# Kernel optimization log

Measured on AMD Instinct MI355X. Metric: run time of the kernel, lower is better.

The kernel has to match this reference:

```python
import jax, jax.numpy as jnp
import numpy as np

N_NODES = 100000


def _gcn_layer(x, W, b, src, dst, n):
    # PyG GCNConv with default add_self_loops=True, symmetric normalization.
    h = x @ W  # [N, out]
    deg = jax.ops.segment_sum(jnp.ones_like(dst, dtype=h.dtype), dst, num_segments=n)
    dinv = jnp.where(deg > 0, jax.lax.rsqrt(deg), 0.0)
    norm = dinv[src] * dinv[dst]  # [E]
    msg = h[src] * norm[:, None]  # gather + scale
    out = jax.ops.segment_sum(msg, dst, num_segments=n)  # scatter-add at targets
    return out + b


def setup_inputs() -> dict:
    key = jax.random.key(0)
    ks = jax.random.split(key, 8)
    n, e = N_NODES, 3200000
    x = jax.random.normal(ks[0], (n, 16), dtype=jnp.float32)
    edge_index = jax.random.randint(ks[1], (2, e), 0, n, dtype=jnp.int64)
    def glorot(k, fi, fo):
        lim = float(np.sqrt(6.0 / (fi + fo)))
        return jax.random.uniform(k, (fi, fo), jnp.float32, -lim, lim)
    return {
        "x": x,
        "edge_index": edge_index,
        "W1": glorot(ks[2], 16, 32), "b1": jnp.zeros((32,), jnp.float32),
        "W2": glorot(ks[3], 32, 64), "b2": jnp.zeros((64,), jnp.float32),
        "W3": glorot(ks[4], 64, 1),  "b3": jnp.zeros((1,), jnp.float32),
    }


def reference(x, edge_index, W1, b1, W2, b2, W3, b3):
    n = x.shape[0]
    # add self-loops once (shared by all layers)
    loops = jnp.arange(n, dtype=edge_index.dtype)
    src = jnp.concatenate([edge_index[0], loops])
    dst = jnp.concatenate([edge_index[1], loops])
    h = _gcn_layer(x, W1, b1, src, dst, n)
    h = jax.nn.relu(h)  # dropout is identity in eval mode
    h = _gcn_layer(h, W2, b2, src, dst, n)
    h = jax.nn.relu(h)
    h = _gcn_layer(h, W3, b3, src, dst, n)
    return jax.nn.sigmoid(h)
```

## Files before the change

kernel.cpp:

```cpp
#include <hip/hip_runtime.h>
#include <hip/hip_bf16.h>
#include <math.h>


#define CW    128
#define CSH   7
#define MAXBUK 1024
#define EPB   8192
#define CAP   5120

static inline int cdiv(int a, int b) { return (a + b - 1) / b; }

__device__ inline unsigned int bf16_rn(float f) {
    unsigned int u = __float_as_uint(f);
    return (u + 0x7fffu + ((u >> 16) & 1u)) >> 16;
}
#define BLO(u) __uint_as_float((u) << 16)
#define BHI(u) __uint_as_float((u) & 0xffff0000u)

#define UNPACK_ADD(A, V) \
    A[0] += BLO(V.x); A[1] += BHI(V.x); \
    A[2] += BLO(V.y); A[3] += BHI(V.y); \
    A[4] += BLO(V.z); A[5] += BHI(V.z); \
    A[6] += BLO(V.w); A[7] += BHI(V.w);
#define UNPACK_ADD2(A, V) \
    A[0] += BLO(V.x); A[1] += BHI(V.x); \
    A[2] += BLO(V.y); A[3] += BHI(V.y);


__global__ void __launch_bounds__(256) k_bscatter(const int* __restrict__ src,
                                                  const int* __restrict__ dst,
                                                  int* __restrict__ gcur,
                                                  int* __restrict__ ebuf, int e, int nbuk) {
    __shared__ int lh[MAXBUK];
    __shared__ int lo[MAXBUK];
    __shared__ int lb[MAXBUK];
    __shared__ int sh[256];
    __shared__ int stage[EPB];
    __shared__ unsigned short bkOf[EPB];
    int4 db[8];
    int t = threadIdx.x;
    for (int b = t; b < nbuk; b += 256) lh[b] = 0;
    __syncthreads();
    int base4 = blockIdx.x * (EPB / 4);
    int e4 = e >> 2;
#pragma unroll
    for (int j = 0; j < 8; j++) {
        int i4 = base4 + j * 256 + t;
        if (i4 < e4) {
            int4 d = ((const int4*)dst)[i4];
            db[j] = d;
            atomicAdd(&lh[d.x >> CSH], 1); atomicAdd(&lh[d.y >> CSH], 1);
            atomicAdd(&lh[d.z >> CSH], 1); atomicAdd(&lh[d.w >> CSH], 1);
        } else db[j] = make_int4(-1, -1, -1, -1);
    }
    __syncthreads();
    int carry = 0;
    for (int cb = 0; cb < nbuk; cb += 256) {
        int b = cb + t;
        int c = (b < nbuk) ? lh[b] : 0;
        if (b < nbuk && c) lb[b] = b * CAP + atomicAdd(&gcur[b], c);
        sh[t] = c;
        __syncthreads();
        for (int o = 1; o < 256; o <<= 1) {
            int u = (t >= o) ? sh[t - o] : 0;
            __syncthreads();
            sh[t] += u;
            __syncthreads();
        }
        if (b < nbuk) lo[b] = sh[t] - c + carry;
        carry += sh[255];
        __syncthreads();
    }
    for (int b = t; b < nbuk; b += 256) lh[b] = 0;
    __syncthreads();
#pragma unroll
    for (int j = 0; j < 8; j++) {
        int i4 = base4 + j * 256 + t;
        if (i4 < e4) {
            int4 s = ((const int4*)src)[i4];
            int4 d = db[j];
            int dd, ss, b, r, slot;
#define PUT(DX, SX) \
            dd = DX; ss = SX; b = dd >> CSH; \
            r = atomicAdd(&lh[b], 1); slot = lo[b] + r; \
            stage[slot] = ((dd & (CW - 1)) << 17) | ss; \
            bkOf[slot] = (unsigned short)b;
            PUT(d.x, s.x) PUT(d.y, s.y) PUT(d.z, s.z) PUT(d.w, s.w)
#undef PUT
        }
    }
    __syncthreads();
    int tot = min(EPB, e - blockIdx.x * EPB);
#pragma unroll
    for (int j = 0; j < 32; j++) {
        int slot = j * 256 + t;
        if (slot < tot) {
            int b = bkOf[slot];
            ebuf[lb[b] + (slot - lo[b])] = stage[slot];
        }
    }
}


__global__ void __launch_bounds__(512) k_csr2(const int* __restrict__ ebuf,
                                              const int* __restrict__ gcur,
                                              int* __restrict__ rowstart,
                                              int* __restrict__ csr_src,
                                              float* __restrict__ dinv,
                                              const float* __restrict__ x,
                                              unsigned int* __restrict__ xs,
                                              int n, int e, int nbuk) {
    __shared__ int cnt[CW];
    __shared__ int offs[CW];
    __shared__ int red[512];
    int t = threadIdx.x;
    int bid = blockIdx.x;
    int part = 0;
    for (int j = t; j < bid; j += 512) part += gcur[j];
    red[t] = part;
    __syncthreads();
    for (int o = 256; o > 0; o >>= 1) {
        if (t < o) red[t] += red[t + o];
        __syncthreads();
    }
    int dbeg = red[0];
    if (t < CW) cnt[t] = 0;
    __syncthreads();
    int cnt_b = gcur[bid];
    const int4* eb4 = (const int4*)(ebuf + (size_t)bid * CAP);
    int n4 = (cnt_b + 3) >> 2;
    for (int k4 = t; k4 < n4; k4 += 512) {
        int4 v = eb4[k4];
        int rem = cnt_b - (k4 << 2);
        atomicAdd(&cnt[v.x >> 17], 1);
        if (rem > 1) atomicAdd(&cnt[v.y >> 17], 1);
        if (rem > 2) atomicAdd(&cnt[v.z >> 17], 1);
        if (rem > 3) atomicAdd(&cnt[v.w >> 17], 1);
    }
    __syncthreads();
    int v = (t < CW) ? cnt[t] : 0;
    if (t < CW) offs[t] = v;
    __syncthreads();
    for (int o = 1; o < CW; o <<= 1) {
        int u = (t < CW && t >= o) ? offs[t - o] : 0;
        __syncthreads();
        if (t < CW) offs[t] += u;
        __syncthreads();
    }
    int node = bid * CW + t;
    if (t < CW) {
        int ex = offs[t] - v;
        float dd = rsqrtf((float)v + 1.0f);
        if (node < n) {
            rowstart[node] = dbeg + ex;
            dinv[node] = dd;
            const float4* xr = (const float4*)(x + (size_t)node * 16);
            float4 v0 = xr[0], v1 = xr[1], v2 = xr[2], v3 = xr[3];
            uint4 o0, o1;
            o0.x = bf16_rn(v0.x * dd) | (bf16_rn(v0.y * dd) << 16);
            o0.y = bf16_rn(v0.z * dd) | (bf16_rn(v0.w * dd) << 16);
            o0.z = bf16_rn(v1.x * dd) | (bf16_rn(v1.y * dd) << 16);
            o0.w = bf16_rn(v1.z * dd) | (bf16_rn(v1.w * dd) << 16);
            o1.x = bf16_rn(v2.x * dd) | (bf16_rn(v2.y * dd) << 16);
            o1.y = bf16_rn(v2.z * dd) | (bf16_rn(v2.w * dd) << 16);
            o1.z = bf16_rn(v3.x * dd) | (bf16_rn(v3.y * dd) << 16);
            o1.w = bf16_rn(v3.z * dd) | (bf16_rn(v3.w * dd) << 16);
            uint4* xo = (uint4*)(xs + (size_t)node * 8);
            xo[0] = o0; xo[1] = o1;
        }
        cnt[t] = ex;
    }
    __syncthreads();
    for (int k4 = t; k4 < n4; k4 += 512) {
        int4 vv = eb4[k4];
        int rem = cnt_b - (k4 << 2);
        int pv, r;
#define SCAT(PV) pv = PV; r = atomicAdd(&cnt[pv >> 17], 1); csr_src[dbeg + r] = pv & 0x1FFFF;
        SCAT(vv.x)
        if (rem > 1) { SCAT(vv.y) }
        if (rem > 2) { SCAT(vv.z) }
        if (rem > 3) { SCAT(vv.w) }
#undef SCAT
    }
    if (bid == 0 && t == 0) rowstart[n] = e;
}


__global__ void __launch_bounds__(256) k_pull16d(const int* __restrict__ rowstart,
                                                 const int* __restrict__ csr_src,
                                                 const float* __restrict__ dinv,
                                                 const unsigned int* __restrict__ xs,
                                                 const float* __restrict__ W1,
                                                 const float* __restrict__ b1,
                                                 unsigned int* __restrict__ h1s, int n) {
    __shared__ float sAgg[4][16];
    __shared__ float sDd[4];
    int t = threadIdx.x;
    int wv = t >> 6;
    int lane = t & 63;
    int wid = blockIdx.x * 4 + wv;
    if (wid < n) {
        int q = lane & 3;
        int beg = rowstart[wid], end = rowstart[wid + 1];
        const uint2* x2 = (const uint2*)xs;
        float dd = dinv[wid];
        uint2 sv = x2[(size_t)wid * 4 + q];
        float a0[4], a1[4], a2[4];
#pragma unroll
        for (int i = 0; i < 4; i++) { a0[i] = 0.f; a1[i] = 0.f; a2[i] = 0.f; }
        int k = beg + (lane >> 2);
        for (; k + 32 < end; k += 48) {
            int s0 = __builtin_nontemporal_load(csr_src + k);
            int s1 = __builtin_nontemporal_load(csr_src + k + 16);
            int s2 = __builtin_nontemporal_load(csr_src + k + 32);
            uint2 v0 = x2[(size_t)s0 * 4 + q];
            uint2 v1 = x2[(size_t)s1 * 4 + q];
            uint2 v2 = x2[(size_t)s2 * 4 + q];
            UNPACK_ADD2(a0, v0);
            UNPACK_ADD2(a1, v1);
            UNPACK_ADD2(a2, v2);
        }
        for (; k < end; k += 16) {
            int s0 = __builtin_nontemporal_load(csr_src + k);
            uint2 v0 = x2[(size_t)s0 * 4 + q];
            UNPACK_ADD2(a0, v0);
        }
#pragma unroll
        for (int i = 0; i < 4; i++) a0[i] += a1[i] + a2[i];
#pragma unroll
        for (int off = 4; off < 64; off <<= 1)
#pragma unroll
            for (int i = 0; i < 4; i++) a0[i] += __shfl_xor(a0[i], off);
        UNPACK_ADD2(a0, sv);
        if (lane < 4) {
#pragma unroll
            for (int i = 0; i < 4; i++) sAgg[wv][q * 4 + i] = a0[i] * dd;
            if (q == 0) sDd[wv] = dd;
        }
    }
    __syncthreads();
    if (t < 64) {
        int w2 = t >> 4, c = t & 15;
        int node = blockIdx.x * 4 + w2;
        if (node < n) {
            float dd = sDd[w2];
            const float* a = sAgg[w2];
            float o0 = b1[2 * c], o1 = b1[2 * c + 1];
#pragma unroll
            for (int k = 0; k < 16; k++) {
                float av = a[k];
                o0 += av * W1[k * 32 + 2 * c];
                o1 += av * W1[k * 32 + 2 * c + 1];
            }
            h1s[(size_t)node * 16 + c] =
                bf16_rn(fmaxf(o0, 0.f) * dd) | (bf16_rn(fmaxf(o1, 0.f) * dd) << 16);
        }
    }
}


__global__ void __launch_bounds__(256) k_pull32(const int* __restrict__ rowstart,
                                                const int* __restrict__ csr_src,
                                                const float* __restrict__ dinv,
                                                const unsigned int* __restrict__ h1s,
                                                float* __restrict__ agg32, int n) {
    int wid = (blockIdx.x * blockDim.x + threadIdx.x) >> 6;
    if (wid >= n) return;
    int lane = threadIdx.x & 63;
    int f4 = lane & 3;
    int beg = rowstart[wid], end = rowstart[wid + 1];
    const uint4* h4 = (const uint4*)h1s;
    float dd = dinv[wid];
    uint4 sv = h4[(size_t)wid * 4 + f4];
    float acc[8], ac1[8], ac2[8];
#pragma unroll
    for (int i = 0; i < 8; i++) { acc[i] = 0.f; ac1[i] = 0.f; ac2[i] = 0.f; }
    int k = beg + (lane >> 2);
    for (; k + 32 < end; k += 48) {
        int s0 = __builtin_nontemporal_load(csr_src + k);
        int s1 = __builtin_nontemporal_load(csr_src + k + 16);
        int s2 = __builtin_nontemporal_load(csr_src + k + 32);
        uint4 v0 = h4[(size_t)s0 * 4 + f4];
        uint4 v1 = h4[(size_t)s1 * 4 + f4];
        uint4 v2 = h4[(size_t)s2 * 4 + f4];
        UNPACK_ADD(acc, v0);
        UNPACK_ADD(ac1, v1);
        UNPACK_ADD(ac2, v2);
    }
    for (; k < end; k += 16) {
        int s0 = __builtin_nontemporal_load(csr_src + k);
        uint4 v0 = h4[(size_t)s0 * 4 + f4];
        UNPACK_ADD(acc, v0);
    }
#pragma unroll
    for (int i = 0; i < 8; i++) acc[i] += ac1[i] + ac2[i];
#pragma unroll
    for (int off = 4; off < 64; off <<= 1)
#pragma unroll
        for (int i = 0; i < 8; i++) acc[i] += __shfl_xor(acc[i], off);
    UNPACK_ADD(acc, sv);
    if (lane < 4) {
        float4* o4 = (float4*)(agg32 + (size_t)wid * 32 + f4 * 8);
        o4[0] = make_float4(acc[0] * dd, acc[1] * dd, acc[2] * dd, acc[3] * dd);
        o4[1] = make_float4(acc[4] * dd, acc[5] * dd, acc[6] * dd, acc[7] * dd);
    }
}


__global__ void __launch_bounds__(256) k_dense2(const float* __restrict__ agg,
                                                const float* __restrict__ dinv,
                                                const float* __restrict__ W2,
                                                const float* __restrict__ b2,
                                                const float* __restrict__ W3,
                                                float* __restrict__ t2, int n) {
    int node = blockIdx.x * 256 + threadIdx.x;
    if (node >= n) return;
    float in[32];
    const float4* a4 = (const float4*)(agg + (size_t)node * 32);
#pragma unroll
    for (int f = 0; f < 8; f++) {
        float4 v = a4[f];
        in[4 * f] = v.x; in[4 * f + 1] = v.y; in[4 * f + 2] = v.z; in[4 * f + 3] = v.w;
    }
    float p = 0.f;
#pragma unroll
    for (int cb = 0; cb < 4; cb++) {
        float o[16];
#pragma unroll
        for (int c = 0; c < 16; c++) o[c] = b2[cb * 16 + c];
#pragma unroll
        for (int k = 0; k < 32; k++) {
            float ik = in[k];
#pragma unroll
            for (int c = 0; c < 16; c++) o[c] += ik * W2[k * 64 + cb * 16 + c];
        }
#pragma unroll
        for (int c = 0; c < 16; c++) p += fmaxf(o[c], 0.f) * W3[cb * 16 + c];
    }
    t2[node] = p * dinv[node];
}


__global__ void __launch_bounds__(256) k_pull1_sig(const int* __restrict__ rowstart,
                                                   const int* __restrict__ csr_src,
                                                   const float* __restrict__ dinv,
                                                   const float* __restrict__ t2,
                                                   const float* __restrict__ b3,
                                                   float* __restrict__ out, int n) {
    int tid = blockIdx.x * blockDim.x + threadIdx.x;
    int wid = tid >> 5;
    if (wid >= n) return;
    int lane32 = threadIdx.x & 31;
    int beg = rowstart[wid], end = rowstart[wid + 1];
    float selfv = t2[wid];
    float dd = dinv[wid];
    float acc = 0.f, ac1 = 0.f;
    int k = beg + lane32;
    for (; k + 32 < end; k += 64) {
        acc += t2[__builtin_nontemporal_load(csr_src + k)];
        ac1 += t2[__builtin_nontemporal_load(csr_src + k + 32)];
    }
    if (k < end) acc += t2[__builtin_nontemporal_load(csr_src + k)];
    acc += ac1;
#pragma unroll
    for (int off = 1; off < 32; off <<= 1) acc += __shfl_xor(acc, off);
    if (lane32 == 0) {
        float v = (acc + selfv) * dd + b3[0];
        out[wid] = 1.0f / (1.0f + expf(-v));
    }
}


extern "C" void kernel_launch(void* const* d_in, const int* in_sizes, int n_in,
                              void* d_out, int out_size, void* d_ws, size_t ws_size,
                              hipStream_t stream) {
    const float* x  = (const float*)d_in[0];
    const int*   ei = (const int*)d_in[1];
    const float* W1 = (const float*)d_in[2];
    const float* b1 = (const float*)d_in[3];
    const float* W2 = (const float*)d_in[4];
    const float* b2 = (const float*)d_in[5];
    const float* W3 = (const float*)d_in[6];
    const float* b3 = (const float*)d_in[7];

    const int n = in_sizes[0] / 16;
    const int e = in_sizes[1] / 2;
    const int* src = ei;
    const int* dst = ei + e;
    const int nbuk = cdiv(n, CW);

    auto rup = [](size_t v) { return (v + 15) & ~(size_t)15; };
    char* wp = (char*)d_ws;
    auto alloc = [&](size_t elems) { void* p = wp; wp += rup(elems) * 4; return p; };
    int*   gcur     = (int*)  alloc(MAXBUK);
    float* dinv     = (float*)alloc(n);
    int*   rowstart = (int*)  alloc(n + 1);
    int*   ebuf     = (int*)  alloc((size_t)nbuk * CAP);
    int*   csr_src  = (int*)  alloc(e);
    unsigned int* xs  = (unsigned int*)alloc((size_t)8 * n);
    unsigned int* h1s = (unsigned int*)alloc((size_t)16 * n);
    float* agg32    = (float*)alloc((size_t)32 * n);
    float* t2       = (float*)alloc(n);

    float* out = (float*)d_out;
    const int B = 256;

    hipMemsetAsync(gcur, 0, MAXBUK * 4, stream);
    k_bscatter<<<cdiv(e, EPB), B, 0, stream>>>(src, dst, gcur, ebuf, e, nbuk);
    k_csr2<<<nbuk, 512, 0, stream>>>(ebuf, gcur, rowstart, csr_src,
                                     dinv, x, xs, n, e, nbuk);

    k_pull16d<<<cdiv(n, 4), B, 0, stream>>>(rowstart, csr_src, dinv, xs, W1, b1, h1s, n);

    k_pull32<<<cdiv(n * 64, B), B, 0, stream>>>(rowstart, csr_src, dinv, h1s, agg32, n);
    k_dense2<<<cdiv(n, B), B, 0, stream>>>(agg32, dinv, W2, b2, W3, t2, n);

    k_pull1_sig<<<cdiv(n * 32, B), B, 0, stream>>>(rowstart, csr_src, dinv, t2, b3, out, n);
}
```

Baseline: 215.6 us.

## Fuse layer-2 gather with dense W2/W3 projection in one kernel

Merges the 32-wide neighbour aggregation kernel and the dense layer-2/W3 projection kernel into one. Each wavefront aggregates one node, puts the result in shared memory, then has each lane compute one of the 64 outputs and reduce across the wave with shuffles. This removes the fp32 agg32 intermediate round trip through global memory and one launch. It also cuts the gather unroll from three accumulators to two, and adds a block-wide barrier plus a cross-lane reduction per node.

```diff
diff --git a/kernel.cpp b/kernel.cpp
--- a/kernel.cpp
+++ b/kernel.cpp
@@ -260,85 +260,67 @@
 }
 
 
-__global__ void __launch_bounds__(256) k_pull32(const int* __restrict__ rowstart,
-                                                const int* __restrict__ csr_src,
-                                                const float* __restrict__ dinv,
-                                                const unsigned int* __restrict__ h1s,
-                                                float* __restrict__ agg32, int n) {
-    int wid = (blockIdx.x * blockDim.x + threadIdx.x) >> 6;
-    if (wid >= n) return;
-    int lane = threadIdx.x & 63;
-    int f4 = lane & 3;
-    int beg = rowstart[wid], end = rowstart[wid + 1];
-    const uint4* h4 = (const uint4*)h1s;
-    float dd = dinv[wid];
-    uint4 sv = h4[(size_t)wid * 4 + f4];
-    float acc[8], ac1[8], ac2[8];
-#pragma unroll
-    for (int i = 0; i < 8; i++) { acc[i] = 0.f; ac1[i] = 0.f; ac2[i] = 0.f; }
-    int k = beg + (lane >> 2);
-    for (; k + 32 < end; k += 48) {
-        int s0 = __builtin_nontemporal_load(csr_src + k);
-        int s1 = __builtin_nontemporal_load(csr_src + k + 16);
-        int s2 = __builtin_nontemporal_load(csr_src + k + 32);
-        uint4 v0 = h4[(size_t)s0 * 4 + f4];
-        uint4 v1 = h4[(size_t)s1 * 4 + f4];
-        uint4 v2 = h4[(size_t)s2 * 4 + f4];
-        UNPACK_ADD(acc, v0);
-        UNPACK_ADD(ac1, v1);
-        UNPACK_ADD(ac2, v2);
-    }
-    for (; k < end; k += 16) {
-        int s0 = __builtin_nontemporal_load(csr_src + k);
-        uint4 v0 = h4[(size_t)s0 * 4 + f4];
-        UNPACK_ADD(acc, v0);
-    }
-#pragma unroll
-    for (int i = 0; i < 8; i++) acc[i] += ac1[i] + ac2[i];
-#pragma unroll
-    for (int off = 4; off < 64; off <<= 1)
-#pragma unroll
-        for (int i = 0; i < 8; i++) acc[i] += __shfl_xor(acc[i], off);
-    UNPACK_ADD(acc, sv);
-    if (lane < 4) {
-        float4* o4 = (float4*)(agg32 + (size_t)wid * 32 + f4 * 8);
-        o4[0] = make_float4(acc[0] * dd, acc[1] * dd, acc[2] * dd, acc[3] * dd);
-        o4[1] = make_float4(acc[4] * dd, acc[5] * dd, acc[6] * dd, acc[7] * dd);
-    }
-}
-
-
-__global__ void __launch_bounds__(256) k_dense2(const float* __restrict__ agg,
-                                                const float* __restrict__ dinv,
-                                                const float* __restrict__ W2,
-                                                const float* __restrict__ b2,
-                                                const float* __restrict__ W3,
-                                                float* __restrict__ t2, int n) {
-    int node = blockIdx.x * 256 + threadIdx.x;
-    if (node >= n) return;
-    float in[32];
-    const float4* a4 = (const float4*)(agg + (size_t)node * 32);
-#pragma unroll
-    for (int f = 0; f < 8; f++) {
-        float4 v = a4[f];
-        in[4 * f] = v.x; in[4 * f + 1] = v.y; in[4 * f + 2] = v.z; in[4 * f + 3] = v.w;
-    }
-    float p = 0.f;
-#pragma unroll
-    for (int cb = 0; cb < 4; cb++) {
-        float o[16];
-#pragma unroll
-        for (int c = 0; c < 16; c++) o[c] = b2[cb * 16 + c];
-#pragma unroll
-        for (int k = 0; k < 32; k++) {
-            float ik = in[k];
-#pragma unroll
-            for (int c = 0; c < 16; c++) o[c] += ik * W2[k * 64 + cb * 16 + c];
-        }
-#pragma unroll
-        for (int c = 0; c < 16; c++) p += fmaxf(o[c], 0.f) * W3[cb * 16 + c];
-    }
-    t2[node] = p * dinv[node];
+__global__ void __launch_bounds__(256) k_pull32f(const int* __restrict__ rowstart,
+                                                 const int* __restrict__ csr_src,
+                                                 const float* __restrict__ dinv,
+                                                 const unsigned int* __restrict__ h1s,
+                                                 const float* __restrict__ W2,
+                                                 const float* __restrict__ b2,
+                                                 const float* __restrict__ W3,
+                                                 float* __restrict__ t2, int n) {
+    __shared__ float sAgg[4][32];
+    __shared__ float sDd[4];
+    int t = threadIdx.x;
+    int wv = t >> 6;
+    int lane = t & 63;
+    int wid = blockIdx.x * 4 + wv;
+    if (wid < n) {
+        int f4 = lane & 3;
+        int beg = rowstart[wid], end = rowstart[wid + 1];
+        const uint4* h4 = (const uint4*)h1s;
+        float dd = dinv[wid];
+        uint4 sv = h4[(size_t)wid * 4 + f4];
+        float acc[8], ac1[8];
+#pragma unroll
+        for (int i = 0; i < 8; i++) { acc[i] = 0.f; ac1[i] = 0.f; }
+        int k = beg + (lane >> 2);
+        for (; k + 16 < end; k += 32) {
+            int s0 = __builtin_nontemporal_load(csr_src + k);
+            int s1 = __builtin_nontemporal_load(csr_src + k + 16);
+            uint4 v0 = h4[(size_t)s0 * 4 + f4];
+            uint4 v1 = h4[(size_t)s1 * 4 + f4];
+            UNPACK_ADD(acc, v0);
+            UNPACK_ADD(ac1, v1);
+        }
+        if (k < end) {
+            int s0 = __builtin_nontemporal_load(csr_src + k);
+            uint4 v0 = h4[(size_t)s0 * 4 + f4];
+            UNPACK_ADD(acc, v0);
+        }
+#pragma unroll
+        for (int i = 0; i < 8; i++) acc[i] += ac1[i];
+#pragma unroll
+        for (int off = 4; off < 64; off <<= 1)
+#pragma unroll
+            for (int i = 0; i < 8; i++) acc[i] += __shfl_xor(acc[i], off);
+        UNPACK_ADD(acc, sv);
+        if (lane < 4) {
+#pragma unroll
+            for (int i = 0; i < 8; i++) sAgg[wv][f4 * 8 + i] = acc[i] * dd;
+            if (f4 == 0) sDd[wv] = dd;
+        }
+    }
+    __syncthreads();
+    if (wid < n) {
+        const float* a = sAgg[wv];
+        float o = b2[lane];
+#pragma unroll
+        for (int k = 0; k < 32; k++) o += a[k] * W2[k * 64 + lane];
+        float p = fmaxf(o, 0.f) * W3[lane];
+#pragma unroll
+        for (int off = 1; off < 64; off <<= 1) p += __shfl_xor(p, off);
+        if (lane == 0) t2[wid] = p * sDd[wv];
+    }
 }
 
 
@@ -400,7 +382,6 @@
     int*   csr_src  = (int*)  alloc(e);
     unsigned int* xs  = (unsigned int*)alloc((size_t)8 * n);
     unsigned int* h1s = (unsigned int*)alloc((size_t)16 * n);
-    float* agg32    = (float*)alloc((size_t)32 * n);
     float* t2       = (float*)alloc(n);
 
     float* out = (float*)d_out;
@@ -413,8 +394,8 @@
 
     k_pull16d<<<cdiv(n, 4), B, 0, stream>>>(rowstart, csr_src, dinv, xs, W1, b1, h1s, n);
 
-    k_pull32<<<cdiv(n * 64, B), B, 0, stream>>>(rowstart, csr_src, dinv, h1s, agg32, n);
-    k_dense2<<<cdiv(n, B), B, 0, stream>>>(agg32, dinv, W2, b2, W3, t2, n);
+    k_pull32f<<<cdiv(n, 4), B, 0, stream>>>(rowstart, csr_src, dinv, h1s,
+                                            W2, b2, W3, t2, n);
 
     k_pull1_sig<<<cdiv(n * 32, B), B, 0, stream>>>(rowstart, csr_src, dinv, t2, b3, out, n);
 }
```

Measured after the change: 196.6 us. -8.8%, faster.
